# Optimization experiments

Measured on AMD Instinct MI355X. Metric: run time of the kernel, lower is better.

The kernel has to match this reference:

```python
import jax, jax.numpy as jnp
import numpy as np
import math

B, H, S, D = 8, 16, 1024, 64

def setup_inputs() -> dict:
    key = jax.random.key(0)
    kq, kk, kv = jax.random.split(key, 3)
    Q = jax.random.normal(kq, (B, H, S, D), dtype=jnp.float32)
    K = jax.random.normal(kk, (B, H, S, D), dtype=jnp.float32)
    V = jax.random.normal(kv, (B, H, S, D), dtype=jnp.float32)
    return {"Q": Q, "K": K, "V": V}

def reference(Q, K, V):
    d_k = K.shape[-1]
    # [B,H,S,S] attention scores
    score = jnp.einsum('bhqd,bhkd->bhqk', Q, K) / math.sqrt(d_k)
    attn = jax.nn.softmax(score, axis=-1)
    return jnp.einsum('bhqk,bhkd->bhqd', attn, V)
```

## Files before the change

kernel.cpp:

```cpp
#include <hip/hip_runtime.h>
#include <hip/hip_bf16.h>
#include <math.h>


#define S_ 1024
#define D_ 64
#define BQ 128
#define KVT 64
#define NTILE (S_ / KVT)
#define TILE_SHORTS (KVT * D_)

typedef __attribute__((ext_vector_type(8))) short bf16x8;
typedef __attribute__((ext_vector_type(4))) float f32x4;

#if __has_builtin(__builtin_amdgcn_exp2f)
#define EXP2F(x) __builtin_amdgcn_exp2f(x)
#else
#define EXP2F(x) exp2f(x)
#endif

__device__ __forceinline__ short f2bf(float f) {
    union { __hip_bfloat16 h; short s; } u;
    u.h = __float2bfloat16(f);
    return u.s;
}

__device__ __forceinline__ void gl2lds16(const short* g, short* l) {
    __builtin_amdgcn_global_load_lds(
        (const __attribute__((address_space(1))) unsigned int*)g,
        (__attribute__((address_space(3))) unsigned int*)l, 16, 0, 0);
}

__device__ __forceinline__ unsigned int pkbf(float a, float b) {
    unsigned int ua = __float_as_uint(a) + 0x8000u;
    unsigned int ub = __float_as_uint(b) + 0x8000u;
    return __builtin_amdgcn_perm(ub, ua, 0x07060302u);
}

__launch_bounds__(256)
__global__ void prepass_kernel(const float* __restrict__ K, const float* __restrict__ V,
                               short* __restrict__ Kb, short* __restrict__ Vb) {
    __shared__ __align__(16) short VtL[D_][72];
    const int tile = blockIdx.x, bh = blockIdx.y;
    const int tid = threadIdx.x;
    const int kv0 = tile * KVT;
    const size_t base = (size_t)bh * (S_ * D_);
    const float* Kp = K + base;
    const float* Vp = V + base;
    short* Kt = Kb + ((size_t)bh * NTILE + tile) * TILE_SHORTS;
    short* Vt = Vb + ((size_t)bh * NTILE + tile) * TILE_SHORTS;

    {
        const int c4 = tid & 15, g = tid >> 4;
        #pragma unroll
        for (int i = 0; i < 2; ++i) {
            const int kp = g + 16 * i;
            #pragma unroll
            for (int j = 0; j < 4; ++j) {
                const int d = c4 + 16 * j;
                float v0 = Vp[(size_t)(kv0 + 2 * kp) * D_ + d];
                float v1 = Vp[(size_t)(kv0 + 2 * kp + 1) * D_ + d];
                short2 vs; vs.x = f2bf(v0); vs.y = f2bf(v1);
                *(short2*)&VtL[d][2 * kp] = vs;
            }
        }
    }
    #pragma unroll
    for (int i = 0; i < 2; ++i) {
        const int s = tid + i * 256;
        const int mb = s >> 7, c = (s >> 6) & 1, lane = s & 63;
        const int quad = lane >> 4, l16 = lane & 15;
        const float* src = Kp + (size_t)(kv0 + mb * 16 + l16) * D_ + c * 32 + quad * 8;
        float4 a = *(const float4*)src;
        float4 b = *(const float4*)(src + 4);
        bf16x8 f;
        f[0]=f2bf(a.x); f[1]=f2bf(a.y); f[2]=f2bf(a.z); f[3]=f2bf(a.w);
        f[4]=f2bf(b.x); f[5]=f2bf(b.y); f[6]=f2bf(b.z); f[7]=f2bf(b.w);
        *(bf16x8*)&Kt[s * 8] = f;
    }
    __syncthreads();
    #pragma unroll
    for (int i = 0; i < 2; ++i) {
        const int s = tid + i * 256;
        const int t = s >> 7, c = (s >> 6) & 1, lane = s & 63;
        const int quad = lane >> 4, l16 = lane & 15;
        bf16x8 f = *(const bf16x8*)&VtL[t * 16 + l16][c * 32 + quad * 8];
        *(bf16x8*)&Vt[s * 8] = f;
    }
}

__launch_bounds__(256, 4)
__global__ void sdpa_kernel(const float* __restrict__ Q,
                            const short* __restrict__ Kb,
                            const short* __restrict__ Vb,
                            float* __restrict__ O) {
    __shared__ __align__(16) short Kbuf[2][TILE_SHORTS];
    __shared__ __align__(16) short Vbuf[2][TILE_SHORTS];
    __shared__ __align__(16) short Pfrag[4][1024];

    const int b   = blockIdx.x;
    const int bh  = (b & 7) | ((b >> 6) << 3);
    const int q0  = ((b >> 3) & 7) * BQ;
    const int tid = threadIdx.x;
    const int w = tid >> 6, lane = tid & 63;
    const int quad = lane >> 4, l16 = lane & 15;

    const size_t base = (size_t)bh * (S_ * D_);
    const float* Qp = Q + base;
    float*       Op = O + base;
    const short* Kg = Kb + (size_t)bh * NTILE * TILE_SHORTS;
    const short* Vg = Vb + (size_t)bh * NTILE * TILE_SHORTS;

    const float qs = 0.18033688011112042f;
    bf16x8 qfrag[2][2];
    #pragma unroll
    for (int nb = 0; nb < 2; ++nb) {
        const int qrow = q0 + w * 32 + nb * 16 + l16;
        #pragma unroll
        for (int c = 0; c < 2; ++c) {
            const float* src = Qp + (size_t)qrow * D_ + c * 32 + quad * 8;
            float4 a = *(const float4*)(src);
            float4 bb = *(const float4*)(src + 4);
            bf16x8 f;
            f[0]=f2bf(a.x*qs);  f[1]=f2bf(a.y*qs);  f[2]=f2bf(a.z*qs);  f[3]=f2bf(a.w*qs);
            f[4]=f2bf(bb.x*qs); f[5]=f2bf(bb.y*qs); f[6]=f2bf(bb.z*qs); f[7]=f2bf(bb.w*qs);
            qfrag[nb][c] = f;
        }
    }

    bf16x8 ones;
    #pragma unroll
    for (int i = 0; i < 8; ++i) ones[i] = (short)0x3F80;

    f32x4 l_acc[2];
    f32x4 o_acc[2][4];
    #pragma unroll
    for (int nb = 0; nb < 2; ++nb) {
        l_acc[nb] = (f32x4)0.f;
        #pragma unroll
        for (int t4 = 0; t4 < 4; ++t4)
            o_acc[nb][t4] = (f32x4)0.f;
    }

    auto stage = [&](int buf, int t) {
        const short* kt = Kg + (size_t)t * TILE_SHORTS;
        const short* vt = Vg + (size_t)t * TILE_SHORTS;
        #pragma unroll
        for (int i = 0; i < 2; ++i) {
            const int blk = i * 4 + w;
            gl2lds16(kt + (blk * 64 + lane) * 8, &Kbuf[buf][blk * 512]);
            gl2lds16(vt + (blk * 64 + lane) * 8, &Vbuf[buf][blk * 512]);
        }
    };

    stage(0, 0);
    __syncthreads();
    int cur = 0;

    #pragma unroll 1
    for (int t = 0; t < NTILE; ++t) {
        if (t + 1 < NTILE) stage(cur ^ 1, t + 1);

        f32x4 st[2][4];
        #pragma unroll
        for (int mb = 0; mb < 4; ++mb) {
            bf16x8 kf0 = *(const bf16x8*)&Kbuf[cur][((mb * 2 + 0) * 64 + lane) * 8];
            bf16x8 kf1 = *(const bf16x8*)&Kbuf[cur][((mb * 2 + 1) * 64 + lane) * 8];
            #pragma unroll
            for (int nb = 0; nb < 2; ++nb) {
                f32x4 acc = (f32x4)0.f;
                acc = __builtin_amdgcn_mfma_f32_16x16x32_bf16(kf0, qfrag[nb][0], acc, 0, 0, 0);
                acc = __builtin_amdgcn_mfma_f32_16x16x32_bf16(kf1, qfrag[nb][1], acc, 0, 0, 0);
                st[nb][mb] = acc;
            }
        }

        bf16x8 pf[2][2];
        #pragma unroll
        for (int nb = 0; nb < 2; ++nb) {
            #pragma unroll
            for (int mb = 0; mb < 4; ++mb) {
                float p0 = EXP2F(st[nb][mb][0]);
                float p1 = EXP2F(st[nb][mb][1]);
                float p2 = EXP2F(st[nb][mb][2]);
                float p3 = EXP2F(st[nb][mb][3]);
                uint2 pk;
                pk.x = pkbf(p0, p1);
                pk.y = pkbf(p2, p3);
                const int c  = mb >> 1;
                const int qp = (mb & 1) * 2 + (quad >> 1);
                const int j0 = (quad & 1) * 4;
                *(uint2*)&Pfrag[w][(c * 64 + qp * 16 + l16) * 8 + j0] = pk;
            }
            pf[nb][0] = *(const bf16x8*)&Pfrag[w][(0 * 64 + lane) * 8];
            pf[nb][1] = *(const bf16x8*)&Pfrag[w][(1 * 64 + lane) * 8];
            l_acc[nb] = __builtin_amdgcn_mfma_f32_16x16x32_bf16(pf[nb][0], ones, l_acc[nb], 0, 0, 0);
            l_acc[nb] = __builtin_amdgcn_mfma_f32_16x16x32_bf16(pf[nb][1], ones, l_acc[nb], 0, 0, 0);
        }

        #pragma unroll
        for (int t4 = 0; t4 < 4; ++t4) {
            bf16x8 vf0 = *(const bf16x8*)&Vbuf[cur][((t4 * 2 + 0) * 64 + lane) * 8];
            bf16x8 vf1 = *(const bf16x8*)&Vbuf[cur][((t4 * 2 + 1) * 64 + lane) * 8];
            #pragma unroll
            for (int nb = 0; nb < 2; ++nb) {
                f32x4 acc = o_acc[nb][t4];
                acc = __builtin_amdgcn_mfma_f32_16x16x32_bf16(pf[nb][0], vf0, acc, 0, 0, 0);
                acc = __builtin_amdgcn_mfma_f32_16x16x32_bf16(pf[nb][1], vf1, acc, 0, 0, 0);
                o_acc[nb][t4] = acc;
            }
        }

        __syncthreads();
        cur ^= 1;
    }

    #pragma unroll
    for (int nb = 0; nb < 2; ++nb) {
        #pragma unroll
        for (int r = 0; r < 4; ++r) {
            const float inv = 1.0f / l_acc[nb][r];
            const int row = q0 + w * 32 + nb * 16 + quad * 4 + r;
            #pragma unroll
            for (int t4 = 0; t4 < 4; ++t4)
                Op[(size_t)row * D_ + t4 * 16 + l16] = o_acc[nb][t4][r] * inv;
        }
    }
}

extern "C" void kernel_launch(void* const* d_in, const int* in_sizes, int n_in,
                              void* d_out, int out_size, void* d_ws, size_t ws_size,
                              hipStream_t stream) {
    const float* Q = (const float*)d_in[0];
    const float* K = (const float*)d_in[1];
    const float* V = (const float*)d_in[2];
    float* O = (float*)d_out;

    const size_t tensor_shorts = (size_t)128 * NTILE * TILE_SHORTS;
    short* Kb = (short*)d_ws;
    short* Vb = Kb + tensor_shorts;

    dim3 pgrid(NTILE, 8 * 16);
    prepass_kernel<<<pgrid, dim3(256), 0, stream>>>(K, V, Kb, Vb);

    sdpa_kernel<<<dim3(1024), dim3(256), 0, stream>>>(Q, Kb, Vb, O);
}
```

Before: 166.1 us.

## Double query tile per block to reuse K/V tiles across more rows

Each block now handles 256 query rows instead of 128, with every wave owning 64 rows (4 row blocks). K and V fragments are loaded from LDS once per tile and reused across all four row blocks, and the loop is reorganised so each row block runs QK, exp, row-sum and PV in turn. This halves the grid to 512 blocks and lowers the occupancy target to 2 blocks per SIMD. It cuts K/V staging traffic per query row, at the cost of higher register pressure and fewer blocks relative to the CU count.

```diff
diff --git a/kernel.cpp b/kernel.cpp
--- a/kernel.cpp
+++ b/kernel.cpp
@@ -5,7 +5,7 @@
 
 #define S_ 1024
 #define D_ 64
-#define BQ 128
+#define BQ 256
 #define KVT 64
 #define NTILE (S_ / KVT)
 #define TILE_SHORTS (KVT * D_)
@@ -89,7 +89,7 @@
     }
 }
 
-__launch_bounds__(256, 4)
+__launch_bounds__(256, 2)
 __global__ void sdpa_kernel(const float* __restrict__ Q,
                             const short* __restrict__ Kb,
                             const short* __restrict__ Vb,
@@ -99,8 +99,8 @@
     __shared__ __align__(16) short Pfrag[4][1024];
 
     const int b   = blockIdx.x;
-    const int bh  = (b & 7) | ((b >> 6) << 3);
-    const int q0  = ((b >> 3) & 7) * BQ;
+    const int bh  = (b & 7) | ((b >> 5) << 3);
+    const int q0  = ((b >> 3) & 3) * BQ;
     const int tid = threadIdx.x;
     const int w = tid >> 6, lane = tid & 63;
     const int quad = lane >> 4, l16 = lane & 15;
@@ -112,10 +112,10 @@
     const short* Vg = Vb + (size_t)bh * NTILE * TILE_SHORTS;
 
     const float qs = 0.18033688011112042f;
-    bf16x8 qfrag[2][2];
-    #pragma unroll
-    for (int nb = 0; nb < 2; ++nb) {
-        const int qrow = q0 + w * 32 + nb * 16 + l16;
+    bf16x8 qfrag[4][2];
+    #pragma unroll
+    for (int nb = 0; nb < 4; ++nb) {
+        const int qrow = q0 + w * 64 + nb * 16 + l16;
         #pragma unroll
         for (int c = 0; c < 2; ++c) {
             const float* src = Qp + (size_t)qrow * D_ + c * 32 + quad * 8;
@@ -132,10 +132,10 @@
     #pragma unroll
     for (int i = 0; i < 8; ++i) ones[i] = (short)0x3F80;
 
-    f32x4 l_acc[2];
-    f32x4 o_acc[2][4];
-    #pragma unroll
-    for (int nb = 0; nb < 2; ++nb) {
+    f32x4 l_acc[4];
+    f32x4 o_acc[4][4];
+    #pragma unroll
+    for (int nb = 0; nb < 4; ++nb) {
         l_acc[nb] = (f32x4)0.f;
         #pragma unroll
         for (int t4 = 0; t4 < 4; ++t4)
@@ -161,29 +161,32 @@
     for (int t = 0; t < NTILE; ++t) {
         if (t + 1 < NTILE) stage(cur ^ 1, t + 1);
 
-        f32x4 st[2][4];
+        bf16x8 kf[4][2], vf[4][2];
         #pragma unroll
         for (int mb = 0; mb < 4; ++mb) {
-            bf16x8 kf0 = *(const bf16x8*)&Kbuf[cur][((mb * 2 + 0) * 64 + lane) * 8];
-            bf16x8 kf1 = *(const bf16x8*)&Kbuf[cur][((mb * 2 + 1) * 64 + lane) * 8];
-            #pragma unroll
-            for (int nb = 0; nb < 2; ++nb) {
+            kf[mb][0] = *(const bf16x8*)&Kbuf[cur][((mb * 2 + 0) * 64 + lane) * 8];
+            kf[mb][1] = *(const bf16x8*)&Kbuf[cur][((mb * 2 + 1) * 64 + lane) * 8];
+            vf[mb][0] = *(const bf16x8*)&Vbuf[cur][((mb * 2 + 0) * 64 + lane) * 8];
+            vf[mb][1] = *(const bf16x8*)&Vbuf[cur][((mb * 2 + 1) * 64 + lane) * 8];
+        }
+
+        #pragma unroll
+        for (int nb = 0; nb < 4; ++nb) {
+            f32x4 st[4];
+            #pragma unroll
+            for (int mb = 0; mb < 4; ++mb) {
                 f32x4 acc = (f32x4)0.f;
-                acc = __builtin_amdgcn_mfma_f32_16x16x32_bf16(kf0, qfrag[nb][0], acc, 0, 0, 0);
-                acc = __builtin_amdgcn_mfma_f32_16x16x32_bf16(kf1, qfrag[nb][1], acc, 0, 0, 0);
-                st[nb][mb] = acc;
-            }
-        }
-
-        bf16x8 pf[2][2];
-        #pragma unroll
-        for (int nb = 0; nb < 2; ++nb) {
+                acc = __builtin_amdgcn_mfma_f32_16x16x32_bf16(kf[mb][0], qfrag[nb][0], acc, 0, 0, 0);
+                acc = __builtin_amdgcn_mfma_f32_16x16x32_bf16(kf[mb][1], qfrag[nb][1], acc, 0, 0, 0);
+                st[mb] = acc;
+            }
+
             #pragma unroll
             for (int mb = 0; mb < 4; ++mb) {
-                float p0 = EXP2F(st[nb][mb][0]);
-                float p1 = EXP2F(st[nb][mb][1]);
-                float p2 = EXP2F(st[nb][mb][2]);
-                float p3 = EXP2F(st[nb][mb][3]);
+                float p0 = EXP2F(st[mb][0]);
+                float p1 = EXP2F(st[mb][1]);
+                float p2 = EXP2F(st[mb][2]);
+                float p3 = EXP2F(st[mb][3]);
                 uint2 pk;
                 pk.x = pkbf(p0, p1);
                 pk.y = pkbf(p2, p3);
@@ -192,21 +195,17 @@
                 const int j0 = (quad & 1) * 4;
                 *(uint2*)&Pfrag[w][(c * 64 + qp * 16 + l16) * 8 + j0] = pk;
             }
-            pf[nb][0] = *(const bf16x8*)&Pfrag[w][(0 * 64 + lane) * 8];
-            pf[nb][1] = *(const bf16x8*)&Pfrag[w][(1 * 64 + lane) * 8];
-            l_acc[nb] = __builtin_amdgcn_mfma_f32_16x16x32_bf16(pf[nb][0], ones, l_acc[nb], 0, 0, 0);
-            l_acc[nb] = __builtin_amdgcn_mfma_f32_16x16x32_bf16(pf[nb][1], ones, l_acc[nb], 0, 0, 0);
-        }
-
-        #pragma unroll
-        for (int t4 = 0; t4 < 4; ++t4) {
-            bf16x8 vf0 = *(const bf16x8*)&Vbuf[cur][((t4 * 2 + 0) * 64 + lane) * 8];
-            bf16x8 vf1 = *(const bf16x8*)&Vbuf[cur][((t4 * 2 + 1) * 64 + lane) * 8];
-            #pragma unroll
-            for (int nb = 0; nb < 2; ++nb) {
+            bf16x8 pf0 = *(const bf16x8*)&Pfrag[w][(0 * 64 + lane) * 8];
+            bf16x8 pf1 = *(const bf16x8*)&Pfrag[w][(1 * 64 + lane) * 8];
+
+            l_acc[nb] = __builtin_amdgcn_mfma_f32_16x16x32_bf16(pf0, ones, l_acc[nb], 0, 0, 0);
+            l_acc[nb] = __builtin_amdgcn_mfma_f32_16x16x32_bf16(pf1, ones, l_acc[nb], 0, 0, 0);
+
+            #pragma unroll
+            for (int t4 = 0; t4 < 4; ++t4) {
                 f32x4 acc = o_acc[nb][t4];
-                acc = __builtin_amdgcn_mfma_f32_16x16x32_bf16(pf[nb][0], vf0, acc, 0, 0, 0);
-                acc = __builtin_amdgcn_mfma_f32_16x16x32_bf16(pf[nb][1], vf1, acc, 0, 0, 0);
+                acc = __builtin_amdgcn_mfma_f32_16x16x32_bf16(pf0, vf[t4][0], acc, 0, 0, 0);
+                acc = __builtin_amdgcn_mfma_f32_16x16x32_bf16(pf1, vf[t4][1], acc, 0, 0, 0);
                 o_acc[nb][t4] = acc;
             }
         }
@@ -216,11 +215,11 @@
     }
 
     #pragma unroll
-    for (int nb = 0; nb < 2; ++nb) {
+    for (int nb = 0; nb < 4; ++nb) {
         #pragma unroll
         for (int r = 0; r < 4; ++r) {
             const float inv = 1.0f / l_acc[nb][r];
-            const int row = q0 + w * 32 + nb * 16 + quad * 4 + r;
+            const int row = q0 + w * 64 + nb * 16 + quad * 4 + r;
             #pragma unroll
             for (int t4 = 0; t4 < 4; ++t4)
                 Op[(size_t)row * D_ + t4 * 16 + l16] = o_acc[nb][t4][r] * inv;
@@ -243,5 +242,5 @@
     dim3 pgrid(NTILE, 8 * 16);
     prepass_kernel<<<pgrid, dim3(256), 0, stream>>>(K, V, Kb, Vb);
 
-    sdpa_kernel<<<dim3(1024), dim3(256), 0, stream>>>(Q, Kb, Vb, O);
-}
+    sdpa_kernel<<<dim3(512), dim3(256), 0, stream>>>(Q, Kb, Vb, O);
+}
```

After: 169.4 us. About the same (+1.9%).
